# Kernel tuning notes

Measured on AMD Instinct MI355X. Metric: run time of the kernel, lower is better.

The kernel has to match this reference:

```python
import jax, jax.numpy as jnp
import numpy as np

B, S, D = 2, 2048, 1024
H, DK = 16, 64          # n_heads, d_kv; inner_dim = H*DK = D
NUM_BUCKETS = 32        # T5 relative_attention_num_buckets
MAX_DIST = 128          # T5 relative_attention_max_distance
SM_SCALE = 1.0 / np.sqrt(H)  # module uses 1/sqrt(n_heads), not 1/sqrt(d_kv)


def setup_inputs() -> dict:
    key = jax.random.key(0)
    ks = jax.random.split(key, 6)
    w = 0.02  # typical init scale for projection weights
    return {
        "hidden_states": jax.random.normal(ks[0], (B, S, D), jnp.float32),
        "Wq": jax.random.normal(ks[1], (D, H * DK), jnp.float32) * w,
        "Wk": jax.random.normal(ks[2], (D, H * DK), jnp.float32) * w,
        "Wv": jax.random.normal(ks[3], (D, H * DK), jnp.float32) * w,
        "Wo": jax.random.normal(ks[4], (H * DK, D), jnp.float32) * w,
        "rel_bias": jax.random.normal(ks[5], (NUM_BUCKETS, H), jnp.float32) * w,
    }


def _relative_position_buckets(qlen, klen):
    """T5 bidirectional relative-position bucketing -> [qlen, klen] int32."""
    ctx = jnp.arange(qlen, dtype=jnp.int32)[:, None]
    mem = jnp.arange(klen, dtype=jnp.int32)[None, :]
    rp = mem - ctx  # relative position
    nb = NUM_BUCKETS // 2  # bidirectional split
    ret = (rp > 0).astype(jnp.int32) * nb
    rpa = jnp.abs(rp)
    max_exact = nb // 2
    is_small = rpa < max_exact
    rpf = jnp.maximum(rpa, 1).astype(jnp.float32)
    large = max_exact + (
        jnp.log(rpf / max_exact) / np.log(MAX_DIST / max_exact) * (nb - max_exact)
    ).astype(jnp.int32)
    large = jnp.minimum(large, nb - 1)
    return ret + jnp.where(is_small, rpa, large)


def reference(hidden_states, Wq, Wk, Wv, Wo, rel_bias):
    b, s, d = hidden_states.shape
    q = (hidden_states @ Wq).reshape(b, s, H, DK)
    k = (hidden_states @ Wk).reshape(b, s, H, DK)
    v = (hidden_states @ Wv).reshape(b, s, H, DK)

    buckets = _relative_position_buckets(s, s)        # [S, S]
    bias = rel_bias[buckets]                          # [S, S, H]
    bias = jnp.transpose(bias, (2, 0, 1))[None]       # [1, H, S, S]

    scores = jnp.einsum("bqhd,bkhd->bhqk", q, k) * SM_SCALE + bias
    attn = jax.nn.softmax(scores, axis=-1)
    out = jnp.einsum("bhqk,bkhd->bqhd", attn, v).reshape(b, s, H * DK)
    return out @ Wo
```

## Files before the change

kernel.cpp:

```cpp
#include <hip/hip_runtime.h>
#include <math.h>


typedef _Float16 f16;
typedef _Float16 f16x4 __attribute__((ext_vector_type(4)));
typedef _Float16 f16x8 __attribute__((ext_vector_type(8)));
typedef float f32x4 __attribute__((ext_vector_type(4)));
typedef float f32x16 __attribute__((ext_vector_type(16)));
typedef unsigned int u32;
typedef u32 u32x4 __attribute__((ext_vector_type(4)));

#define MFMA16(a, b, c) __builtin_amdgcn_mfma_f32_16x16x32_f16((a), (b), (c), 0, 0, 0)
#define MFMA32(a, b, c) __builtin_amdgcn_mfma_f32_32x32x16_f16((a), (b), (c), 0, 0, 0)

static __device__ __forceinline__ float EXP2(float x) {
  float r;
  asm("v_exp_f32 %0, %1" : "=v"(r) : "v"(x));
  return r;
}

static __device__ __forceinline__ u32 pk2(float a, float b) {
  return __builtin_bit_cast(u32, __builtin_amdgcn_cvt_pkrtz(a, b));
}
static __device__ __forceinline__ void swap32(u32& a, u32& b) {
  asm volatile("v_permlane32_swap_b32 %0, %1" : "+v"(a), "+v"(b));
}

#define KEEPV8(v8)                                                        \
  do {                                                                    \
    u32x4 _t = __builtin_bit_cast(u32x4, (v8));                           \
    asm volatile("" ::"v"(_t[0]), "v"(_t[1]), "v"(_t[2]), "v"(_t[3]));    \
  } while (0)

__device__ __forceinline__ void gload16(const f16* g, f16* l) {
  __builtin_amdgcn_global_load_lds(
      (const __attribute__((address_space(1))) void*)g,
      (__attribute__((address_space(3))) void*)l, 16, 0, 0);
}

__global__ void prep_kernel(const float* __restrict__ X, const float* __restrict__ w0,
                            const float* __restrict__ w1, const float* __restrict__ w2,
                            const float* __restrict__ w3, const float* __restrict__ relb,
                            f16x4* __restrict__ xh, f16* __restrict__ wt,
                            f16* __restrict__ bias_rel) {
  const int z = blockIdx.z;
  const int tx = threadIdx.x, ty = threadIdx.y;
  if (z < 4) {
    const float* w = (z == 0) ? w0 : (z == 1) ? w1 : (z == 2) ? w2 : w3;
    float sc = (z == 0) ? 0.36067376022224085f : 1.0f;
    __shared__ float tile[32][33];
    int kt = blockIdx.x * 32, nt = blockIdx.y * 32;
#pragma unroll
    for (int i = 0; i < 4; ++i)
      tile[ty + i * 8][tx] = w[(size_t)(kt + ty + i * 8) * 1024 + nt + tx];
    __syncthreads();
#pragma unroll
    for (int i = 0; i < 4; ++i)
      wt[((size_t)z * 1024 + nt + ty + i * 8) * 1024 + kt + tx] =
          (f16)(tile[tx][ty + i * 8] * sc);
  } else if (z == 4) {
    if (blockIdx.x >= 8) return;
    int idx = (blockIdx.x * 32 + blockIdx.y) * 256 + ty * 32 + tx;
    int h = idx >> 12;
    int r = idx & 4095;
    int rp = r - 2048;
    if (rp < -2047) rp = -2047;
    int bucket = (rp > 0) ? 16 : 0;
    int rpa = (rp < 0) ? -rp : rp;
    if (rpa < 8) {
      bucket += rpa;
    } else {
      int large = 8 + (int)(logf((float)rpa / 8.0f) / logf(16.0f) * 8.0f);
      bucket += (large < 15) ? large : 15;
    }
    bias_rel[idx] = (f16)(relb[bucket * 16 + h] * 1.4426950408889634f);
  } else {
    const float4* x4 = (const float4*)X;
    int i = (blockIdx.x * 32 + blockIdx.y) * 256 + ty * 32 + tx;
#pragma unroll
    for (int rep = 0; rep < 4; ++rep, i += 262144) {
      float4 v = x4[i];
      f16x4 o;
      o[0] = (f16)v.x; o[1] = (f16)v.y; o[2] = (f16)v.z; o[3] = (f16)v.w;
      xh[i] = o;
    }
  }
}

__global__ void transpose_v_kernel(const f16* __restrict__ vin, f16* __restrict__ vout) {
  __shared__ f16 tile[32][33];
  int bh = blockIdx.z;
  int s0 = blockIdx.x * 32, d0 = blockIdx.y * 32;
  int tx = threadIdx.x, ty = threadIdx.y;
  const f16* src = vin + ((size_t)bh * 2048 + s0) * 64 + d0;
#pragma unroll
  for (int i = 0; i < 4; ++i) tile[ty + i * 8][tx] = src[(size_t)(ty + i * 8) * 64 + tx];
  __syncthreads();
  f16* dst = vout + ((size_t)bh * 64 + d0) * 2048 + s0;
#pragma unroll
  for (int i = 0; i < 4; ++i) dst[(size_t)(ty + i * 8) * 2048 + tx] = tile[tx][ty + i * 8];
}

__device__ __forceinline__ void gemm128_core(const f16* __restrict__ A, const f16* __restrict__ Bt,
                                             int mrow, int ncol0, f16* sm ,
                                             f32x4 acc[4][4]) {
  const int t = threadIdx.x;
  const int lane = t & 63, w = t >> 6;
  const int cL = lane & 15, g = lane >> 4;
  const int wr = w >> 1, wc = w & 1;

  const int c0 = w * 128 + lane;
  const int c1 = c0 + 64;
  const int rA0 = c0 >> 2, kA0 = ((c0 & 3) ^ (rA0 & 3)) << 3;
  const int rA1 = c1 >> 2, kA1 = ((c1 & 3) ^ (rA1 & 3)) << 3;
  const f16* gA0 = A + (size_t)(mrow + rA0) * 1024 + kA0;
  const f16* gA1 = A + (size_t)(mrow + rA1) * 1024 + kA1;
  const f16* gB0 = Bt + (size_t)(ncol0 + rA0) * 1024 + kA0;
  const f16* gB1 = Bt + (size_t)(ncol0 + rA1) * 1024 + kA1;
  const int lds0 = (w * 2) * 512, lds1 = (w * 2 + 1) * 512;

#define GSTAGE(buf, k0)                            \
  do {                                             \
    f16* s_ = sm + (buf) * 8192;                   \
    gload16(gA0 + (k0), s_ + lds0);                \
    gload16(gA1 + (k0), s_ + lds1);                \
    gload16(gB0 + (k0), s_ + 4096 + lds0);         \
    gload16(gB1 + (k0), s_ + 4096 + lds1);         \
  } while (0)

  GSTAGE(0, 0);
  __syncthreads();
#pragma unroll 2
  for (int ks = 0; ks < 32; ++ks) {
    const int cur = ks & 1;
    if (ks < 31) GSTAGE(cur ^ 1, (ks + 1) * 32);
    const f16* bA = sm + cur * 8192;
    const f16* bB = bA + 4096;
    f16x8 af[4], bf[4];
#pragma unroll
    for (int m = 0; m < 4; ++m) {
      int r = wr * 64 + m * 16 + cL;
      af[m] = *(const f16x8*)&bA[r * 32 + ((g ^ (r & 3)) << 3)];
    }
#pragma unroll
    for (int n = 0; n < 4; ++n) {
      int r = wc * 64 + n * 16 + cL;
      bf[n] = *(const f16x8*)&bB[r * 32 + ((g ^ (r & 3)) << 3)];
    }
#pragma unroll
    for (int m = 0; m < 4; ++m)
#pragma unroll
      for (int n = 0; n < 4; ++n) acc[m][n] = MFMA16(af[m], bf[n], acc[m][n]);
    __syncthreads();
  }
#undef GSTAGE
}

__global__ __launch_bounds__(256) void gemm_qkv_kernel(const f16* __restrict__ Xh,
                                                       const f16* __restrict__ Wt,
                                                       f16* __restrict__ Qh,
                                                       f16* __restrict__ Kh,
                                                       f16* __restrict__ Vrow) {
  __shared__ __align__(16) f16 sm[2][8192];
  int mrow = blockIdx.y * 128, ncol0 = blockIdx.x * 128;
  f32x4 acc[4][4] = {};
  gemm128_core(Xh, Wt, mrow, ncol0, &sm[0][0], acc);
  int lane = threadIdx.x & 63, w = threadIdx.x >> 6;
  int cL = lane & 15, g = lane >> 4;
  int wr = w >> 1, wc = w & 1;
  int which = (ncol0 + wc * 64) >> 10;
  f16* dst = (which == 0) ? Qh : (which == 1) ? Kh : Vrow;
#pragma unroll
  for (int m = 0; m < 4; ++m) {
#pragma unroll
    for (int n = 0; n < 4; ++n) {
#pragma unroll
      for (int r = 0; r < 4; ++r) {
        int tt = mrow + wr * 64 + m * 16 + g * 4 + r;
        int b = tt >> 11, s = tt & 2047;
        int col = (ncol0 + wc * 64 + n * 16 + cL) & 1023;
        int hh = col >> 6, dk = col & 63;
        dst[(((size_t)b * 16 + hh) * 2048 + s) * 64 + dk] = (f16)acc[m][n][r];
      }
    }
  }
}

__global__ __launch_bounds__(256) void gemm_out_kernel(const f16* __restrict__ Oh,
                                                       const f16* __restrict__ WoT,
                                                       float* __restrict__ out) {
  __shared__ __align__(16) f16 sm[2][8192];
  int mrow = blockIdx.y * 128, ncol0 = blockIdx.x * 128;
  f32x4 acc[4][4] = {};
  gemm128_core(Oh, WoT, mrow, ncol0, &sm[0][0], acc);
  int lane = threadIdx.x & 63, w = threadIdx.x >> 6;
  int cL = lane & 15, g = lane >> 4;
  int wr = w >> 1, wc = w & 1;
#pragma unroll
  for (int m = 0; m < 4; ++m)
#pragma unroll
    for (int n = 0; n < 4; ++n)
#pragma unroll
      for (int r = 0; r < 4; ++r) {
        int tt = mrow + wr * 64 + m * 16 + g * 4 + r;
        out[(size_t)tt * 1024 + ncol0 + wc * 64 + n * 16 + cL] = acc[m][n][r];
      }
}

__global__ __launch_bounds__(512) void attn_kernel(const f16* __restrict__ Qh,
                                                   const f16* __restrict__ Kh,
                                                   const f16* __restrict__ Vt,
                                                   const f16* __restrict__ bias_rel,
                                                   f16* __restrict__ Oh) {
  __shared__ __align__(16) f16 sKV[2][4][8192];
  __shared__ __align__(16) f16 sB[2176];
  const int p = blockIdx.x;
  const int L = ((p & 7) << 6) + (p >> 3);
  const int bh = L >> 4;
  const int qt = (L & 15) << 7;
  const int h = bh & 15, b = bh >> 4;
  int t = threadIdx.x;
  int lane = t & 63, wave = t >> 6;
  const int gr = wave >> 2, sw = wave & 3;
  int lo5 = lane & 31, hi = lane >> 5;
  const size_t bhS = (size_t)bh * 2048;
  const int qrow = qt + sw * 32 + lo5;

  const f16* qp = Qh + (bhS + qrow) * 64 + hi * 8;
  f16x8 qf[4];
#pragma unroll
  for (int m = 0; m < 4; ++m) qf[m] = *(const f16x8*)(qp + 16 * m);

  float cpos = (float)bias_rel[(size_t)h * 4096 + 4095];
  float cneg = (float)bias_rel[(size_t)h * 4096 + 1];

#pragma unroll
  for (int m = 0; m < 4; ++m) KEEPV8(qf[m]);
  asm volatile("" ::"v"(cpos), "v"(cneg));

  {
    const float4* gB = (const float4*)(bias_rel + (size_t)h * 4096 + 1920 - qt);
    for (int i = t; i < 272; i += 512) ((float4*)sB)[i] = gB[i];
  }

  const int tg = t & 255;
  const int rK0 = tg >> 3, ccK0 = ((tg & 7) ^ (rK0 & 7)) << 3;
  const int rK1 = rK0 + 32, ccK1 = ((tg & 7) ^ (rK1 & 7)) << 3;
  const f16* gK0 = Kh + (bhS + rK0) * 64 + ccK0;
  const f16* gK1 = Kh + (bhS + rK1) * 64 + ccK1;
  const f16* gV0 = Vt + ((size_t)bh * 64 + rK0) * 2048 + ccK0;
  const f16* gV1 = Vt + ((size_t)bh * 64 + rK1) * 2048 + ccK1;
  const int ldsA = sw * 512, ldsB = sw * 512 + 2048;

#define ASTAGE(buf, key0)                           \
  do {                                              \
    f16* s_ = &sKV[gr][buf][0];                     \
    gload16(gK0 + (size_t)(key0) * 64, s_ + ldsA);  \
    gload16(gK1 + (size_t)(key0) * 64, s_ + ldsB);  \
    gload16(gV0 + (key0), s_ + 4096 + ldsA);        \
    gload16(gV1 + (key0), s_ + 4096 + ldsB);        \
  } while (0)

  f32x16 o0 = {}, o1 = {};
  float m_ = -INFINITY, lsum = 0.f;
  const int sw7 = lo5 & 7;
  const int kbase = gr << 10;

  auto qk = [&](const f16* kb, f32x16& s0, f32x16& s1) {
    const f16* kr0 = kb + lo5 * 64;
    const f16* kr1 = kb + (32 + lo5) * 64;
#pragma unroll
    for (int m = 0; m < 4; ++m) {
      int c = ((2 * m + hi) ^ sw7) << 3;
      s0 = MFMA32(*(const f16x8*)(kr0 + c), qf[m], s0);
      s1 = MFMA32(*(const f16x8*)(kr1 + c), qf[m], s1);
    }
  };
  auto rowmax = [&](const f32x16& a, const f32x16& bvec) -> float {
    float tm[16];
#pragma unroll
    for (int i = 0; i < 16; ++i) tm[i] = fmaxf(a[i], bvec[i]);
#pragma unroll
    for (int s2 = 8; s2; s2 >>= 1)
#pragma unroll
      for (int i = 0; i < 8; ++i)
        if (i < s2) tm[i] = fmaxf(tm[i], tm[i + s2]);
    return tm[0];
  };
  auto softpack = [&](const f32x16& s0, const f32x16& s1, f16x8& b0, f16x8& b1, f16x8& b2,
                      f16x8& b3) -> float {
    float pr[16];
    u32 w0, w1, w2, w3, w4, w5, w6, w7;
#pragma unroll
    for (int i = 0; i < 16; ++i) pr[i] = EXP2(s0[i] - m_);
    w0 = pk2(pr[0], pr[1]);   w1 = pk2(pr[2], pr[3]);
    w2 = pk2(pr[4], pr[5]);   w3 = pk2(pr[6], pr[7]);
    w4 = pk2(pr[8], pr[9]);   w5 = pk2(pr[10], pr[11]);
    w6 = pk2(pr[12], pr[13]); w7 = pk2(pr[14], pr[15]);
#pragma unroll
    for (int s2 = 8; s2; s2 >>= 1)
#pragma unroll
      for (int i = 0; i < 8; ++i)
        if (i < s2) pr[i] += pr[i + s2];
    float ls = pr[0];
    swap32(w0, w2); swap32(w1, w3); swap32(w4, w6); swap32(w5, w7);
    b0 = __builtin_bit_cast(f16x8, (u32x4){w0, w1, w2, w3});
    b1 = __builtin_bit_cast(f16x8, (u32x4){w4, w5, w6, w7});
#pragma unroll
    for (int i = 0; i < 16; ++i) pr[i] = EXP2(s1[i] - m_);
    w0 = pk2(pr[0], pr[1]);   w1 = pk2(pr[2], pr[3]);
    w2 = pk2(pr[4], pr[5]);   w3 = pk2(pr[6], pr[7]);
    w4 = pk2(pr[8], pr[9]);   w5 = pk2(pr[10], pr[11]);
    w6 = pk2(pr[12], pr[13]); w7 = pk2(pr[14], pr[15]);
#pragma unroll
    for (int s2 = 8; s2; s2 >>= 1)
#pragma unroll
      for (int i = 0; i < 8; ++i)
        if (i < s2) pr[i] += pr[i + s2];
    ls += pr[0];
    swap32(w0, w2); swap32(w1, w3); swap32(w4, w6); swap32(w5, w7);
    b2 = __builtin_bit_cast(f16x8, (u32x4){w0, w1, w2, w3});
    b3 = __builtin_bit_cast(f16x8, (u32x4){w4, w5, w6, w7});
    return ls;
  };
  auto pv = [&](const f16* vb, const f16x8& b0, const f16x8& b1, const f16x8& b2,
                const f16x8& b3) {
    const f16* vr0 = vb + lo5 * 64;
    const f16* vr1 = vb + (32 + lo5) * 64;
    {
      int c = ((0 + hi) ^ sw7) << 3;
      o0 = MFMA32(*(const f16x8*)(vr0 + c), b0, o0);
      o1 = MFMA32(*(const f16x8*)(vr1 + c), b0, o1);
    }
    {
      int c = ((2 + hi) ^ sw7) << 3;
      o0 = MFMA32(*(const f16x8*)(vr0 + c), b1, o0);
      o1 = MFMA32(*(const f16x8*)(vr1 + c), b1, o1);
    }
    {
      int c = ((4 + hi) ^ sw7) << 3;
      o0 = MFMA32(*(const f16x8*)(vr0 + c), b2, o0);
      o1 = MFMA32(*(const f16x8*)(vr1 + c), b2, o1);
    }
    {
      int c = ((6 + hi) ^ sw7) << 3;
      o0 = MFMA32(*(const f16x8*)(vr0 + c), b3, o0);
      o1 = MFMA32(*(const f16x8*)(vr1 + c), b3, o1);
    }
  };
  auto biasinit = [&](int key0, f32x16& s0, f32x16& s1) {
    const int dkt = key0 - qt;
    if (dkt >= 256 || dkt <= -192) {
      float c = (dkt > 0) ? cpos : cneg;
#pragma unroll
      for (int i = 0; i < 16; ++i) { s0[i] = c; s1[i] = c; }
    } else {
      const int bb = key0 + 4 * hi - sw * 32 - lo5 + 128;
#pragma unroll
      for (int i = 0; i < 16; ++i) {
        int pat = (i & 3) + 8 * (i >> 2);
        s0[i] = (float)sB[bb + pat];
        s1[i] = (float)sB[bb + 32 + pat];
      }
    }
  };

  ASTAGE(0, kbase);
  ASTAGE(1, kbase + 64);
  asm volatile("s_waitcnt lgkmcnt(0)" ::: "memory");

  for (int pp = 0; pp < 8; ++pp) {
    asm volatile("s_waitcnt vmcnt(0)" ::: "memory");
    __builtin_amdgcn_s_barrier();
    if (pp < 7) {
      ASTAGE((2 * pp + 2) & 3, kbase + (2 * pp + 2) * 64);
      ASTAGE((2 * pp + 3) & 3, kbase + (2 * pp + 3) * 64);
    }
    const int keyA = kbase + 2 * pp * 64;
    const f16* bufA = &sKV[gr][(2 * pp) & 3][0];
    const f16* bufB = &sKV[gr][(2 * pp + 1) & 3][0];

    f32x16 saA0, saA1, saB0, saB1;
    biasinit(keyA, saA0, saA1);
    biasinit(keyA + 64, saB0, saB1);
    __builtin_amdgcn_s_setprio(1);
    qk(bufA, saA0, saA1);
    qk(bufB, saB0, saB1);
    __builtin_amdgcn_s_setprio(0);

    float mx = fmaxf(rowmax(saA0, saA1), rowmax(saB0, saB1));
    mx = fmaxf(mx, __shfl_xor(mx, 32));
    if (__any(mx > m_ + 8.f)) {
      float mn = fmaxf(m_, mx);
      float corr = EXP2(m_ - mn);
      lsum *= corr;
      m_ = mn;
#pragma unroll
      for (int i = 0; i < 16; ++i) { o0[i] *= corr; o1[i] *= corr; }
    }

    f16x8 f0, f1, f2, f3;
    lsum += softpack(saA0, saA1, f0, f1, f2, f3);
    __builtin_amdgcn_s_setprio(1);
    pv(bufA + 4096, f0, f1, f2, f3);
    __builtin_amdgcn_s_setprio(0);
    lsum += softpack(saB0, saB1, f0, f1, f2, f3);
    __builtin_amdgcn_s_setprio(1);
    pv(bufB + 4096, f0, f1, f2, f3);
    __builtin_amdgcn_s_setprio(0);
  }
#undef ASTAGE

  __syncthreads();
  float* sX = (float*)&sKV[0][0][0];
  const int slot = (sw * 64 + lane) * 35;
  if (gr == 1) {
#pragma unroll
    for (int i = 0; i < 16; ++i) {
      sX[slot + i] = o0[i];
      sX[slot + 16 + i] = o1[i];
    }
    sX[slot + 32] = m_;
    sX[slot + 33] = lsum;
  }
  __syncthreads();
  if (gr == 0) {
    float m2 = sX[slot + 32], l2 = sX[slot + 33];
    float mn = fmaxf(m_, m2);
    float c1 = EXP2(m_ - mn), c2 = EXP2(m2 - mn);
    float s = lsum * c1 + l2 * c2;
    s += __shfl_xor(s, 32);
    float inv = 1.0f / s;
    size_t base = ((size_t)b * 2048 + qrow) * 1024 + h * 64 + 4 * hi;
#pragma unroll
    for (int rq = 0; rq < 4; ++rq) {
      f16x4 v0, v1;
#pragma unroll
      for (int j = 0; j < 4; ++j) {
        v0[j] = (f16)((o0[rq * 4 + j] * c1 + sX[slot + rq * 4 + j] * c2) * inv);
        v1[j] = (f16)((o1[rq * 4 + j] * c1 + sX[slot + 16 + rq * 4 + j] * c2) * inv);
      }
      *(f16x4*)&Oh[base + 8 * rq] = v0;
      *(f16x4*)&Oh[base + 32 + 8 * rq] = v1;
    }
  }
}


extern "C" void kernel_launch(void* const* d_in, const int* in_sizes, int n_in,
                              void* d_out, int out_size, void* d_ws, size_t ws_size,
                              hipStream_t stream) {
  const float* X = (const float*)d_in[0];
  const float* Wq = (const float*)d_in[1];
  const float* Wk = (const float*)d_in[2];
  const float* Wv = (const float*)d_in[3];
  const float* Wo = (const float*)d_in[4];
  const float* relb = (const float*)d_in[5];

  const size_t MB8 = (size_t)8 << 20;
  if (ws_size < 6 * MB8 + (1 << 19)) return;

  char* ws = (char*)d_ws;
  f16* Xh = (f16*)(ws + 0 * MB8);
  f16* Wt = (f16*)(ws + 1 * MB8);
  f16* Qh = (f16*)(ws + 2 * MB8);
  f16* Kh = (f16*)(ws + 3 * MB8);
  f16* Vt = (f16*)(ws + 4 * MB8);
  f16* Oh = (f16*)(ws + 5 * MB8);
  f16* brel = (f16*)(ws + 6 * MB8);
  f16* Vrow = Oh;

  prep_kernel<<<dim3(32, 32, 6), dim3(32, 8), 0, stream>>>(X, Wq, Wk, Wv, Wo, relb,
                                                           (f16x4*)Xh, Wt, brel);
  gemm_qkv_kernel<<<dim3(24, 32), dim3(256), 0, stream>>>(Xh, Wt, Qh, Kh, Vrow);
  transpose_v_kernel<<<dim3(64, 2, 32), dim3(32, 8), 0, stream>>>(Vrow, Vt);
  attn_kernel<<<dim3(512), dim3(512), 0, stream>>>(Qh, Kh, Vt, brel, Oh);
  gemm_out_kernel<<<dim3(8, 32), dim3(256), 0, stream>>>(Oh, Wt + (size_t)3072 * 1024,
                                                         (float*)d_out);
}
```

Baseline: 136.2 us.

## Give each wave two query tiles and split keys across four wave groups

Each wave now handles 64 query rows as two 32-row tiles that share every K and V fragment loaded from LDS, so each shared-memory read feeds twice as many MFMAs. The key range is split four ways across wave groups instead of two, and the LDS pipeline drops from four stages to double buffering of 64-key tiles. The final merge combines three partial softmax states through shared memory. The cost is more accumulator and Q registers per wave, a shallower prefetch pipeline and a longer merge epilogue.

```diff
diff --git a/kernel.cpp b/kernel.cpp
--- a/kernel.cpp
+++ b/kernel.cpp
@@ -212,7 +212,7 @@
                                                    const f16* __restrict__ Vt,
                                                    const f16* __restrict__ bias_rel,
                                                    f16* __restrict__ Oh) {
-  __shared__ __align__(16) f16 sKV[2][4][8192];
+  __shared__ __align__(16) f16 sKV[4][2][8192];
   __shared__ __align__(16) f16 sB[2176];
   const int p = blockIdx.x;
   const int L = ((p & 7) << 6) + (p >> 3);
@@ -221,21 +221,28 @@
   const int h = bh & 15, b = bh >> 4;
   int t = threadIdx.x;
   int lane = t & 63, wave = t >> 6;
-  const int gr = wave >> 2, sw = wave & 3;
+  const int gr = wave >> 1, sw = wave & 1;
   int lo5 = lane & 31, hi = lane >> 5;
   const size_t bhS = (size_t)bh * 2048;
-  const int qrow = qt + sw * 32 + lo5;
-
-  const f16* qp = Qh + (bhS + qrow) * 64 + hi * 8;
-  f16x8 qf[4];
-#pragma unroll
-  for (int m = 0; m < 4; ++m) qf[m] = *(const f16x8*)(qp + 16 * m);
+  const int qbase = qt + sw * 64;
+
+  const f16* qpA = Qh + (bhS + qbase + lo5) * 64 + hi * 8;
+  const f16* qpB = qpA + 32 * 64;
+  f16x8 qfA[4], qfB[4];
+#pragma unroll
+  for (int m = 0; m < 4; ++m) {
+    qfA[m] = *(const f16x8*)(qpA + 16 * m);
+    qfB[m] = *(const f16x8*)(qpB + 16 * m);
+  }
 
   float cpos = (float)bias_rel[(size_t)h * 4096 + 4095];
   float cneg = (float)bias_rel[(size_t)h * 4096 + 1];
 
 #pragma unroll
-  for (int m = 0; m < 4; ++m) KEEPV8(qf[m]);
+  for (int m = 0; m < 4; ++m) {
+    KEEPV8(qfA[m]);
+    KEEPV8(qfB[m]);
+  }
   asm volatile("" ::"v"(cpos), "v"(cneg));
 
   {
@@ -243,39 +250,31 @@
     for (int i = t; i < 272; i += 512) ((float4*)sB)[i] = gB[i];
   }
 
-  const int tg = t & 255;
-  const int rK0 = tg >> 3, ccK0 = ((tg & 7) ^ (rK0 & 7)) << 3;
-  const int rK1 = rK0 + 32, ccK1 = ((tg & 7) ^ (rK1 & 7)) << 3;
-  const f16* gK0 = Kh + (bhS + rK0) * 64 + ccK0;
-  const f16* gK1 = Kh + (bhS + rK1) * 64 + ccK1;
-  const f16* gV0 = Vt + ((size_t)bh * 64 + rK0) * 2048 + ccK0;
-  const f16* gV1 = Vt + ((size_t)bh * 64 + rK1) * 2048 + ccK1;
-  const int ldsA = sw * 512, ldsB = sw * 512 + 2048;
-
-#define ASTAGE(buf, key0)                           \
-  do {                                              \
-    f16* s_ = &sKV[gr][buf][0];                     \
-    gload16(gK0 + (size_t)(key0) * 64, s_ + ldsA);  \
-    gload16(gK1 + (size_t)(key0) * 64, s_ + ldsB);  \
-    gload16(gV0 + (key0), s_ + 4096 + ldsA);        \
-    gload16(gV1 + (key0), s_ + 4096 + ldsB);        \
+  const int tg = t & 127;
+  const int r0 = tg >> 3;
+  const int cc = ((tg & 7) ^ (r0 & 7)) << 3;
+  const f16* gK0 = Kh + (bhS + r0) * 64 + cc;
+  const f16* gV0 = Vt + ((size_t)bh * 64 + r0) * 2048 + cc;
+  const int ldsK = sw * 512;
+
+#define ASTAGE(buf, key0)                                        \
+  do {                                                           \
+    f16* s_ = &sKV[gr][buf][0];                                  \
+    gload16(gK0 + (size_t)((key0) + 0) * 64, s_ + ldsK);         \
+    gload16(gK0 + (size_t)((key0) + 16) * 64, s_ + ldsK + 1024); \
+    gload16(gK0 + (size_t)((key0) + 32) * 64, s_ + ldsK + 2048); \
+    gload16(gK0 + (size_t)((key0) + 48) * 64, s_ + ldsK + 3072); \
+    gload16(gV0 + (key0), s_ + 4096 + ldsK);                     \
+    gload16(gV0 + (key0) + 32768, s_ + 4096 + ldsK + 1024);      \
+    gload16(gV0 + (key0) + 65536, s_ + 4096 + ldsK + 2048);      \
+    gload16(gV0 + (key0) + 98304, s_ + 4096 + ldsK + 3072);      \
   } while (0)
 
-  f32x16 o0 = {}, o1 = {};
-  float m_ = -INFINITY, lsum = 0.f;
+  f32x16 o0A = {}, o1A = {}, o0B = {}, o1B = {};
+  float mA = -INFINITY, mB = -INFINITY, lsA = 0.f, lsB = 0.f;
   const int sw7 = lo5 & 7;
-  const int kbase = gr << 10;
-
-  auto qk = [&](const f16* kb, f32x16& s0, f32x16& s1) {
-    const f16* kr0 = kb + lo5 * 64;
-    const f16* kr1 = kb + (32 + lo5) * 64;
-#pragma unroll
-    for (int m = 0; m < 4; ++m) {
-      int c = ((2 * m + hi) ^ sw7) << 3;
-      s0 = MFMA32(*(const f16x8*)(kr0 + c), qf[m], s0);
-      s1 = MFMA32(*(const f16x8*)(kr1 + c), qf[m], s1);
-    }
-  };
+  const int kbase = gr << 9;
+
   auto rowmax = [&](const f32x16& a, const f32x16& bvec) -> float {
     float tm[16];
 #pragma unroll
@@ -285,14 +284,14 @@
 #pragma unroll
       for (int i = 0; i < 8; ++i)
         if (i < s2) tm[i] = fmaxf(tm[i], tm[i + s2]);
-    return tm[0];
+    return fmaxf(tm[0], __shfl_xor(tm[0], 32));
   };
-  auto softpack = [&](const f32x16& s0, const f32x16& s1, f16x8& b0, f16x8& b1, f16x8& b2,
-                      f16x8& b3) -> float {
+  auto softpack = [&](const f32x16& s0, const f32x16& s1, float mm, f16x8& b0, f16x8& b1,
+                      f16x8& b2, f16x8& b3) -> float {
     float pr[16];
     u32 w0, w1, w2, w3, w4, w5, w6, w7;
 #pragma unroll
-    for (int i = 0; i < 16; ++i) pr[i] = EXP2(s0[i] - m_);
+    for (int i = 0; i < 16; ++i) pr[i] = EXP2(s0[i] - mm);
     w0 = pk2(pr[0], pr[1]);   w1 = pk2(pr[2], pr[3]);
     w2 = pk2(pr[4], pr[5]);   w3 = pk2(pr[6], pr[7]);
     w4 = pk2(pr[8], pr[9]);   w5 = pk2(pr[10], pr[11]);
@@ -307,7 +306,7 @@
     b0 = __builtin_bit_cast(f16x8, (u32x4){w0, w1, w2, w3});
     b1 = __builtin_bit_cast(f16x8, (u32x4){w4, w5, w6, w7});
 #pragma unroll
-    for (int i = 0; i < 16; ++i) pr[i] = EXP2(s1[i] - m_);
+    for (int i = 0; i < 16; ++i) pr[i] = EXP2(s1[i] - mm);
     w0 = pk2(pr[0], pr[1]);   w1 = pk2(pr[2], pr[3]);
     w2 = pk2(pr[4], pr[5]);   w3 = pk2(pr[6], pr[7]);
     w4 = pk2(pr[8], pr[9]);   w5 = pk2(pr[10], pr[11]);
@@ -323,125 +322,156 @@
     b3 = __builtin_bit_cast(f16x8, (u32x4){w4, w5, w6, w7});
     return ls;
   };
-  auto pv = [&](const f16* vb, const f16x8& b0, const f16x8& b1, const f16x8& b2,
-                const f16x8& b3) {
+
+  ASTAGE(0, kbase);
+  asm volatile("s_waitcnt lgkmcnt(0)" ::: "memory");
+
+  for (int it = 0; it < 8; ++it) {
+    asm volatile("s_waitcnt vmcnt(0)" ::: "memory");
+    __builtin_amdgcn_s_barrier();
+    if (it < 7) ASTAGE((it + 1) & 1, kbase + (it + 1) * 64);
+
+    const int key0 = kbase + it * 64;
+    const f16* kb = &sKV[gr][it & 1][0];
+    const f16* vb = kb + 4096;
+    const int dkt = key0 - qt;
+
+    f32x16 saA0, saA1, saB0, saB1;
+    if (dkt >= 256 || dkt <= -192) {
+      float c = (dkt > 0) ? cpos : cneg;
+#pragma unroll
+      for (int i = 0; i < 16; ++i) { saA0[i] = c; saA1[i] = c; saB0[i] = c; saB1[i] = c; }
+    } else {
+      const int bbA = key0 + 4 * hi - sw * 64 - lo5 + 128;
+#pragma unroll
+      for (int i = 0; i < 16; ++i) {
+        int pat = (i & 3) + 8 * (i >> 2);
+        float t0 = (float)sB[bbA + pat];
+        saA0[i] = t0;
+        saB1[i] = t0;
+        saA1[i] = (float)sB[bbA + 32 + pat];
+        saB0[i] = (float)sB[bbA - 32 + pat];
+      }
+    }
+    const f16* kr0 = kb + lo5 * 64;
+    const f16* kr1 = kb + (32 + lo5) * 64;
+    f16x8 k0[4], k1[4];
+#pragma unroll
+    for (int m = 0; m < 4; ++m) {
+      int c = ((2 * m + hi) ^ sw7) << 3;
+      k0[m] = *(const f16x8*)(kr0 + c);
+      k1[m] = *(const f16x8*)(kr1 + c);
+    }
+    __builtin_amdgcn_s_setprio(1);
+#pragma unroll
+    for (int m = 0; m < 4; ++m) {
+      saA0 = MFMA32(k0[m], qfA[m], saA0);
+      saA1 = MFMA32(k1[m], qfA[m], saA1);
+      saB0 = MFMA32(k0[m], qfB[m], saB0);
+      saB1 = MFMA32(k1[m], qfB[m], saB1);
+    }
+    __builtin_amdgcn_s_setprio(0);
+    float mxA = rowmax(saA0, saA1);
+    float mxB = rowmax(saB0, saB1);
+    if (__any((mxA > mA + 8.f) || (mxB > mB + 8.f))) {
+      float mnA = fmaxf(mA, mxA), mnB = fmaxf(mB, mxB);
+      float cA = EXP2(mA - mnA), cB = EXP2(mB - mnB);
+      lsA *= cA; lsB *= cB;
+      mA = mnA; mB = mnB;
+#pragma unroll
+      for (int i = 0; i < 16; ++i) {
+        o0A[i] *= cA; o1A[i] *= cA; o0B[i] *= cB; o1B[i] *= cB;
+      }
+    }
     const f16* vr0 = vb + lo5 * 64;
     const f16* vr1 = vb + (32 + lo5) * 64;
-    {
-      int c = ((0 + hi) ^ sw7) << 3;
-      o0 = MFMA32(*(const f16x8*)(vr0 + c), b0, o0);
-      o1 = MFMA32(*(const f16x8*)(vr1 + c), b0, o1);
-    }
-    {
-      int c = ((2 + hi) ^ sw7) << 3;
-      o0 = MFMA32(*(const f16x8*)(vr0 + c), b1, o0);
-      o1 = MFMA32(*(const f16x8*)(vr1 + c), b1, o1);
-    }
-    {
-      int c = ((4 + hi) ^ sw7) << 3;
-      o0 = MFMA32(*(const f16x8*)(vr0 + c), b2, o0);
-      o1 = MFMA32(*(const f16x8*)(vr1 + c), b2, o1);
-    }
-    {
-      int c = ((6 + hi) ^ sw7) << 3;
-      o0 = MFMA32(*(const f16x8*)(vr0 + c), b3, o0);
-      o1 = MFMA32(*(const f16x8*)(vr1 + c), b3, o1);
-    }
-  };
-  auto biasinit = [&](int key0, f32x16& s0, f32x16& s1) {
-    const int dkt = key0 - qt;
-    if (dkt >= 256 || dkt <= -192) {
-      float c = (dkt > 0) ? cpos : cneg;
-#pragma unroll
-      for (int i = 0; i < 16; ++i) { s0[i] = c; s1[i] = c; }
-    } else {
-      const int bb = key0 + 4 * hi - sw * 32 - lo5 + 128;
-#pragma unroll
-      for (int i = 0; i < 16; ++i) {
-        int pat = (i & 3) + 8 * (i >> 2);
-        s0[i] = (float)sB[bb + pat];
-        s1[i] = (float)sB[bb + 32 + pat];
-      }
-    }
-  };
-
-  ASTAGE(0, kbase);
-  ASTAGE(1, kbase + 64);
-  asm volatile("s_waitcnt lgkmcnt(0)" ::: "memory");
-
-  for (int pp = 0; pp < 8; ++pp) {
-    asm volatile("s_waitcnt vmcnt(0)" ::: "memory");
-    __builtin_amdgcn_s_barrier();
-    if (pp < 7) {
-      ASTAGE((2 * pp + 2) & 3, kbase + (2 * pp + 2) * 64);
-      ASTAGE((2 * pp + 3) & 3, kbase + (2 * pp + 3) * 64);
-    }
-    const int keyA = kbase + 2 * pp * 64;
-    const f16* bufA = &sKV[gr][(2 * pp) & 3][0];
-    const f16* bufB = &sKV[gr][(2 * pp + 1) & 3][0];
-
-    f32x16 saA0, saA1, saB0, saB1;
-    biasinit(keyA, saA0, saA1);
-    biasinit(keyA + 64, saB0, saB1);
+    f16x8 v0[4], v1[4];
+#pragma unroll
+    for (int x = 0; x < 4; ++x) {
+      int c = ((2 * x + hi) ^ sw7) << 3;
+      v0[x] = *(const f16x8*)(vr0 + c);
+      v1[x] = *(const f16x8*)(vr1 + c);
+    }
+    f16x8 f0, f1, f2, f3;
+    lsA += softpack(saA0, saA1, mA, f0, f1, f2, f3);
     __builtin_amdgcn_s_setprio(1);
-    qk(bufA, saA0, saA1);
-    qk(bufB, saB0, saB1);
+    o0A = MFMA32(v0[0], f0, o0A); o1A = MFMA32(v1[0], f0, o1A);
+    o0A = MFMA32(v0[1], f1, o0A); o1A = MFMA32(v1[1], f1, o1A);
+    o0A = MFMA32(v0[2], f2, o0A); o1A = MFMA32(v1[2], f2, o1A);
+    o0A = MFMA32(v0[3], f3, o0A); o1A = MFMA32(v1[3], f3, o1A);
     __builtin_amdgcn_s_setprio(0);
-
-    float mx = fmaxf(rowmax(saA0, saA1), rowmax(saB0, saB1));
-    mx = fmaxf(mx, __shfl_xor(mx, 32));
-    if (__any(mx > m_ + 8.f)) {
-      float mn = fmaxf(m_, mx);
-      float corr = EXP2(m_ - mn);
-      lsum *= corr;
-      m_ = mn;
-#pragma unroll
-      for (int i = 0; i < 16; ++i) { o0[i] *= corr; o1[i] *= corr; }
-    }
-
-    f16x8 f0, f1, f2, f3;
-    lsum += softpack(saA0, saA1, f0, f1, f2, f3);
+    lsB += softpack(saB0, saB1, mB, f0, f1, f2, f3);
     __builtin_amdgcn_s_setprio(1);
-    pv(bufA + 4096, f0, f1, f2, f3);
-    __builtin_amdgcn_s_setprio(0);
-    lsum += softpack(saB0, saB1, f0, f1, f2, f3);
-    __builtin_amdgcn_s_setprio(1);
-    pv(bufB + 4096, f0, f1, f2, f3);
+    o0B = MFMA32(v0[0], f0, o0B); o1B = MFMA32(v1[0], f0, o1B);
+    o0B = MFMA32(v0[1], f1, o0B); o1B = MFMA32(v1[1], f1, o1B);
+    o0B = MFMA32(v0[2], f2, o0B); o1B = MFMA32(v1[2], f2, o1B);
+    o0B = MFMA32(v0[3], f3, o0B); o1B = MFMA32(v1[3], f3, o1B);
     __builtin_amdgcn_s_setprio(0);
   }
 #undef ASTAGE
 
   __syncthreads();
   float* sX = (float*)&sKV[0][0][0];
-  const int slot = (sw * 64 + lane) * 35;
-  if (gr == 1) {
+  if (gr > 0) {
+    float* s2 = sX + (size_t)((gr - 1) * 128 + sw * 64 + lane) * 69;
 #pragma unroll
     for (int i = 0; i < 16; ++i) {
-      sX[slot + i] = o0[i];
-      sX[slot + 16 + i] = o1[i];
-    }
-    sX[slot + 32] = m_;
-    sX[slot + 33] = lsum;
+      s2[i] = o0A[i];
+      s2[16 + i] = o1A[i];
+      s2[32 + i] = o0B[i];
+      s2[48 + i] = o1B[i];
+    }
+    s2[64] = mA; s2[65] = lsA; s2[66] = mB; s2[67] = lsB;
   }
   __syncthreads();
   if (gr == 0) {
-    float m2 = sX[slot + 32], l2 = sX[slot + 33];
-    float mn = fmaxf(m_, m2);
-    float c1 = EXP2(m_ - mn), c2 = EXP2(m2 - mn);
-    float s = lsum * c1 + l2 * c2;
-    s += __shfl_xor(s, 32);
-    float inv = 1.0f / s;
-    size_t base = ((size_t)b * 2048 + qrow) * 1024 + h * 64 + 4 * hi;
+#pragma unroll
+    for (int g = 1; g < 4; ++g) {
+      const float* s2 = sX + (size_t)((g - 1) * 128 + sw * 64 + lane) * 69;
+      {
+        float m2 = s2[64], l2 = s2[65];
+        float mn = fmaxf(mA, m2);
+        float c1 = EXP2(mA - mn), c2 = EXP2(m2 - mn);
+#pragma unroll
+        for (int i = 0; i < 16; ++i) {
+          o0A[i] = o0A[i] * c1 + s2[i] * c2;
+          o1A[i] = o1A[i] * c1 + s2[16 + i] * c2;
+        }
+        lsA = lsA * c1 + l2 * c2;
+        mA = mn;
+      }
+      {
+        float m2 = s2[66], l2 = s2[67];
+        float mn = fmaxf(mB, m2);
+        float c1 = EXP2(mB - mn), c2 = EXP2(m2 - mn);
+#pragma unroll
+        for (int i = 0; i < 16; ++i) {
+          o0B[i] = o0B[i] * c1 + s2[32 + i] * c2;
+          o1B[i] = o1B[i] * c1 + s2[48 + i] * c2;
+        }
+        lsB = lsB * c1 + l2 * c2;
+        mB = mn;
+      }
+    }
+    lsA += __shfl_xor(lsA, 32);
+    lsB += __shfl_xor(lsB, 32);
+    float invA = 1.0f / lsA, invB = 1.0f / lsB;
+    size_t baseA = ((size_t)b * 2048 + qbase + lo5) * 1024 + h * 64 + 4 * hi;
+    size_t baseB = baseA + (size_t)32 * 1024;
 #pragma unroll
     for (int rq = 0; rq < 4; ++rq) {
-      f16x4 v0, v1;
+      f16x4 a0, a1, b0, b1;
 #pragma unroll
       for (int j = 0; j < 4; ++j) {
-        v0[j] = (f16)((o0[rq * 4 + j] * c1 + sX[slot + rq * 4 + j] * c2) * inv);
-        v1[j] = (f16)((o1[rq * 4 + j] * c1 + sX[slot + 16 + rq * 4 + j] * c2) * inv);
-      }
-      *(f16x4*)&Oh[base + 8 * rq] = v0;
-      *(f16x4*)&Oh[base + 32 + 8 * rq] = v1;
+        a0[j] = (f16)(o0A[rq * 4 + j] * invA);
+        a1[j] = (f16)(o1A[rq * 4 + j] * invA);
+        b0[j] = (f16)(o0B[rq * 4 + j] * invB);
+        b1[j] = (f16)(o1B[rq * 4 + j] * invB);
+      }
+      *(f16x4*)&Oh[baseA + 8 * rq] = a0;
+      *(f16x4*)&Oh[baseA + 32 + 8 * rq] = a1;
+      *(f16x4*)&Oh[baseB + 8 * rq] = b0;
+      *(f16x4*)&Oh[baseB + 32 + 8 * rq] = b1;
     }
   }
 }
```

Measured after the change: 143.7 us. 1.05x slower.
